# Optimization experiments

Hardware: AMD Instinct MI355X
Metric: run time of the kernel (lower is better)

## Reference

```python
import jax, jax.numpy as jnp
import numpy as np

N_NODES = 100000


def setup_inputs() -> dict:
    key = jax.random.key(0)
    k1, k2, k3, k4, k5 = jax.random.split(key, 5)
    n_edges = 3200000
    in_f, out_f = 256, 256
    X = jax.random.normal(k1, (N_NODES, in_f), dtype=jnp.float32)
    edge_src = jax.random.randint(k2, (n_edges,), 0, N_NODES, dtype=jnp.int32)
    edge_dst = jax.random.randint(k3, (n_edges,), 0, N_NODES, dtype=jnp.int32)
    edge_val = jax.random.uniform(k4, (n_edges,), dtype=jnp.float32)
    # kaiming-uniform-like init for weight (out_f, in_f)
    bound = np.sqrt(6.0 / in_f)
    W = jax.random.uniform(k5, (out_f, in_f), dtype=jnp.float32, minval=-bound, maxval=bound)
    b = jnp.zeros((out_f,), dtype=jnp.float32)
    return {"X": X, "edge_src": edge_src, "edge_dst": edge_dst,
            "edge_val": edge_val, "W": W, "b": b}


def reference(X, edge_src, edge_dst, edge_val, W, b):
    # S = A @ X, where A is COO sparse: A[src, dst] = val
    # gather neighbor features, scale by edge value, scatter-add to src rows
    msgs = edge_val[:, None] * X[edge_dst]              # [E, in_f]
    S = jax.ops.segment_sum(msgs, edge_src, num_segments=N_NODES)  # [N, in_f]
    # dense projection + bias: (A X) W^T + b
    return S @ W.T + b
```

## Files before the change

kernel.cpp:

```cpp
#include <hip/hip_runtime.h>

#define NNODES 100000
#define F 256
#define NBKT ((NNODES + 127) / 128)
#define BKT_CAP 5120
#define CHUNK_A 8192

typedef unsigned short u16;
typedef unsigned int   u32;
typedef __attribute__((ext_vector_type(8))) short short8v;
typedef __attribute__((ext_vector_type(8))) unsigned short ushort8;
typedef __attribute__((ext_vector_type(4))) float f32x4;
typedef __attribute__((ext_vector_type(2))) float f32x2;

#define GLDS(g, l) __builtin_amdgcn_global_load_lds(                                \
    (const __attribute__((address_space(1))) void*)(g),                             \
    (__attribute__((address_space(3))) void*)(l), 16, 0, 0)

__device__ __forceinline__ u16 f2bf(float f) {
    u32 u = __float_as_uint(f);
    u32 r = u + 0x7FFFu + ((u >> 16) & 1u);
    return (u16)(r >> 16);
}

__global__ __launch_bounds__(256) void cast_w_init(const float* __restrict__ W,
                                                   u16* __restrict__ Wb,
                                                   int* __restrict__ cur) {
    int i = blockIdx.x * 256 + threadIdx.x;
    if (i < F * F / 4) {
        float4 w = ((const float4*)W)[i];
        ushort4 o;
        o.x = f2bf(w.x); o.y = f2bf(w.y); o.z = f2bf(w.z); o.w = f2bf(w.w);
        ((ushort4*)Wb)[i] = o;
    }
    if (i < NBKT) cur[i] = i * BKT_CAP;
}

__global__ __launch_bounds__(256) void cast_x(const float* __restrict__ X,
                                              u16* __restrict__ Xb, int total4) {
    int i = blockIdx.x * 256 + threadIdx.x;
    if (i >= total4) return;
    float4 x = ((const float4*)X)[i];
    ushort4 o;
    o.x = f2bf(x.x); o.y = f2bf(x.y); o.z = f2bf(x.z); o.w = f2bf(x.w);
    ((ushort4*)Xb)[i] = o;
}

__global__ __launch_bounds__(256) void gemm_mfma(const u16* __restrict__ Xb,
                                                 const u16* __restrict__ Wb,
                                                 u16* __restrict__ Yb) {
    __shared__ u16 As[128 * 128];
    __shared__ u16 Bs[128 * 128];
    const int tid  = threadIdx.x;
    const int wv   = tid >> 6;
    const int lane = tid & 63;
    const int lm   = lane & 15;
    const int kg   = lane >> 4;
    const int m0   = blockIdx.x * 128;
    const int n0   = blockIdx.y * 128;

    const u32 csb = (u32)(((tid & 15) ^ ((tid >> 4) & 7)) * 16);
    const u32 rbb = (u32)((tid >> 4) * 512);
    const char* gA0 = (const char*)Xb + (size_t)m0 * 512 + rbb + csb;
    const char* gB0 = (const char*)Wb + (size_t)n0 * 512 + rbb + csb;
    const u32 wbase = (u32)(wv * 1024);

    f32x4 acc[2][8];
#pragma unroll
    for (int t = 0; t < 2; ++t)
#pragma unroll
        for (int u = 0; u < 8; ++u) acc[t][u] = (f32x4){0.f, 0.f, 0.f, 0.f};

#pragma unroll
    for (int kt = 0; kt < 2; ++kt) {
        if (kt) __syncthreads();
#pragma unroll
        for (int i = 0; i < 8; ++i) {
            GLDS(gA0 + kt * 256 + i * 8192, (char*)As + i * 4096 + wbase);
            GLDS(gB0 + kt * 256 + i * 8192, (char*)Bs + i * 4096 + wbase);
        }
        __syncthreads();
#pragma unroll
        for (int s = 0; s < 4; ++s) {
            short8v aF[2];
#pragma unroll
            for (int t = 0; t < 2; ++t) {
                int r = wv * 32 + t * 16 + lm;
                int c = (s * 4 + kg) ^ (r & 7);
                aF[t] = *(const short8v*)&As[r * 128 + c * 8];
            }
            short8v bF[8];
#pragma unroll
            for (int u = 0; u < 8; ++u) {
                int r = u * 16 + lm;
                int c = (s * 4 + kg) ^ (r & 7);
                bF[u] = *(const short8v*)&Bs[r * 128 + c * 8];
            }
#pragma unroll
            for (int t = 0; t < 2; ++t)
#pragma unroll
                for (int u = 0; u < 8; ++u)
                    acc[t][u] = __builtin_amdgcn_mfma_f32_16x16x32_bf16(aF[t], bF[u], acc[t][u], 0, 0, 0);
        }
    }

#pragma unroll
    for (int t = 0; t < 2; ++t) {
        int rbase = m0 + wv * 32 + t * 16 + kg * 4;
#pragma unroll
        for (int i = 0; i < 4; ++i) {
            int row = rbase + i;
            if (row < NNODES) {
#pragma unroll
                for (int u = 0; u < 8; ++u)
                    Yb[(size_t)row * F + n0 + u * 16 + lm] = f2bf(acc[t][u][i]);
            }
        }
    }
}

__global__ __launch_bounds__(256) void bin_edges(const int* __restrict__ src,
                                                 const int* __restrict__ dst,
                                                 const float* __restrict__ val,
                                                 int* __restrict__ cur,
                                                 int2* __restrict__ temp,
                                                 int n_edges) {
    __shared__ int hist[NBKT];
    __shared__ int bas[NBKT];
    const int e0 = blockIdx.x * CHUNK_A;
    for (int i = threadIdx.x; i < NBKT; i += 256) hist[i] = 0;
    __syncthreads();

    u32 lpk[32];
#pragma unroll
    for (int k = 0; k < 32; ++k) {
        int e = e0 + k * 256 + threadIdx.x;
        if (e < n_edges) {
            int s = src[e];
            int bkt = s >> 7;
            int l = atomicAdd(&hist[bkt], 1);
            lpk[k] = (u32)l | ((u32)(s & 127) << 13) | ((u32)bkt << 20);
        }
    }
    __syncthreads();
    for (int i = threadIdx.x; i < NBKT; i += 256) {
        int c = hist[i];
        bas[i] = c ? atomicAdd(&cur[i], c) : 0;
    }
    __syncthreads();
#pragma unroll
    for (int k = 0; k < 32; ++k) {
        int e = e0 + k * 256 + threadIdx.x;
        if (e < n_edges) {
            u32 p   = lpk[k];
            int bkt = (int)(p >> 20);
            int pos = bas[bkt] + (int)(p & 0x1FFFu);
            int sl  = (int)((p >> 13) & 127u);
            temp[pos] = make_int2((sl << 20) | dst[e], __float_as_int(val[e]));
        }
    }
}

__global__ __launch_bounds__(256) void sort_bucket(const int* __restrict__ cur,
                                                   const int2* __restrict__ temp,
                                                   int2* __restrict__ pack,
                                                   int2* __restrict__ nodeseg) {
    __shared__ int2 tl[BKT_CAP];
    __shared__ int h[128];
    __shared__ int curl[128];
    const int b = blockIdx.x;
    const int base = b * BKT_CAP;
    int cnt = cur[b] - base;
    if (cnt > BKT_CAP) cnt = BKT_CAP;
    const int tid = threadIdx.x;

    if (tid < 128) h[tid] = 0;
    __syncthreads();
    for (int j = tid; j < cnt; j += 256) {
        int2 t = temp[base + j];
        tl[j] = t;
        atomicAdd(&h[t.x >> 20], 1);
    }
    __syncthreads();
    for (int off = 1; off < 128; off <<= 1) {
        int x = 0;
        if (tid < 128 && tid >= off) x = h[tid - off];
        __syncthreads();
        if (tid < 128) h[tid] += x;
        __syncthreads();
    }
    if (tid < 128) {
        int incl = h[tid];
        int prev = tid ? h[tid - 1] : 0;
        curl[tid] = base + prev;
        int node = b * 128 + tid;
        if (node < NNODES) nodeseg[node] = make_int2(base + prev, base + incl);
    }
    __syncthreads();
    for (int j = tid; j < cnt; j += 256) {
        int2 p = tl[j];
        int loc = p.x >> 20;
        int pos = atomicAdd(&curl[loc], 1);
        pack[pos] = make_int2((p.x & 0xFFFFF) << 9, p.y);
    }
}

__global__ __launch_bounds__(256) void gather_nodes(const int2* __restrict__ nodeseg,
                                                    const int2* __restrict__ pack,
                                                    const u16* __restrict__ Yb,
                                                    const float* __restrict__ bias,
                                                    float* __restrict__ out) {
    int node = blockIdx.x * 4 + (threadIdx.x >> 6);
    if (node >= NNODES) return;
    const int lane = threadIdx.x & 63;
    const int half = lane >> 5;
    const int l5   = lane & 31;
    const u32 loff = (u32)l5 * 16u;
    const char* Ybc = (const char*)Yb;

    int2 seg = nodeseg[node];
    const int beg = seg.x, end = seg.y;

    f32x2 acc2[4];
#pragma unroll
    for (int i = 0; i < 4; ++i) acc2[i] = (f32x2){0.f, 0.f};

    for (int j = beg; j < end; j += 16) {
        u32 off[8];
        float v[8];
        ushort8 y[8];
#pragma unroll
        for (int q = 0; q < 8; ++q) {
            int idx = j + 2 * q + half;
            int safe = idx < end ? idx : end - 1;
            long long raw = __builtin_nontemporal_load((const long long*)&pack[safe]);
            off[q] = (u32)((unsigned long long)raw & 0xFFFFFFFFull);
            v[q] = (idx < end) ? __int_as_float((int)(raw >> 32)) : 0.f;
        }
#pragma unroll
        for (int q = 0; q < 8; ++q)
            y[q] = *(const ushort8*)(Ybc + (off[q] + loff));
#pragma unroll
        for (int q = 0; q < 8; ++q) {
            f32x2 vv; vv[0] = v[q]; vv[1] = v[q];
            const u32* yp = (const u32*)&y[q];
#pragma unroll
            for (int i = 0; i < 4; ++i) {
                u32 pb = yp[i];
                f32x2 yy;
                yy[0] = __uint_as_float(pb << 16);
                yy[1] = __uint_as_float(pb & 0xFFFF0000u);
                acc2[i] = __builtin_elementwise_fma(yy, vv, acc2[i]);
            }
        }
    }

    float acc[8];
#pragma unroll
    for (int i = 0; i < 4; ++i) { acc[2 * i] = acc2[i][0]; acc[2 * i + 1] = acc2[i][1]; }
#pragma unroll
    for (int i = 0; i < 8; ++i) acc[i] += __shfl_xor(acc[i], 32);

    const int col = l5 * 8 + half * 4;
    float4 bv = *(const float4*)&bias[col];
    f32x4 o;
    o[0] = acc[half * 4 + 0] + bv.x;
    o[1] = acc[half * 4 + 1] + bv.y;
    o[2] = acc[half * 4 + 2] + bv.z;
    o[3] = acc[half * 4 + 3] + bv.w;
    __builtin_nontemporal_store(o, (f32x4*)&out[(size_t)node * F + col]);
}

extern "C" void kernel_launch(void* const* d_in, const int* in_sizes, int n_in,
                              void* d_out, int out_size, void* d_ws, size_t ws_size,
                              hipStream_t stream) {
    const float* X        = (const float*)d_in[0];
    const int*   edge_src = (const int*)d_in[1];
    const int*   edge_dst = (const int*)d_in[2];
    const float* edge_val = (const float*)d_in[3];
    const float* W        = (const float*)d_in[4];
    const float* b        = (const float*)d_in[5];
    float*       out      = (float*)d_out;
    const int n_edges     = in_sizes[1];

    char* base = (char*)d_ws;
    const size_t ybBytes   = (size_t)NNODES * F * sizeof(u16);
    const size_t packBytes = (size_t)NBKT * BKT_CAP * sizeof(int2);
    u16*  Yb      = (u16*)base;
    int2* pack    = (int2*)(base + ybBytes);
    int2* temp    = (int2*)(base + ybBytes + packBytes);
    u16*  Xb      = (u16*)pack;
    u16*  Wb      = (u16*)(base + ybBytes + 2 * packBytes);
    int2* nodeseg = (int2*)((char*)Wb + (size_t)F * F * sizeof(u16));
    int*  cur     = (int*)(nodeseg + NNODES);

    cast_w_init<<<(F * F / 4 + 255) / 256, 256, 0, stream>>>(W, Wb, cur);
    int xt4 = NNODES * F / 4;
    cast_x<<<(xt4 + 255) / 256, 256, 0, stream>>>(X, Xb, xt4);

    dim3 ggrid((NNODES + 127) / 128, F / 128);
    gemm_mfma<<<ggrid, 256, 0, stream>>>(Xb, Wb, Yb);

    bin_edges<<<(n_edges + CHUNK_A - 1) / CHUNK_A, 256, 0, stream>>>(edge_src, edge_dst, edge_val,
                                                                     cur, temp, n_edges);
    sort_bucket<<<NBKT, 256, 0, stream>>>(cur, temp, pack, nodeseg);

    gather_nodes<<<(NNODES + 3) / 4, 256, 0, stream>>>(nodeseg, pack, Yb, b, out);
}
```

Baseline: 555.9 us.

## Fuse bucket sort and node gather into one kernel using LDS-resident edges

```diff
diff --git a/kernel.cpp b/kernel.cpp
--- a/kernel.cpp
+++ b/kernel.cpp
@@ -3,7 +3,7 @@
 #define NNODES 100000
 #define F 256
 #define NBKT ((NNODES + 127) / 128)
-#define BKT_CAP 5120
+#define BKT_CAP 5040
 #define CHUNK_A 8192
 
 typedef unsigned short u16;
@@ -156,30 +156,38 @@
             int bkt = (int)(p >> 20);
             int pos = bas[bkt] + (int)(p & 0x1FFFu);
             int sl  = (int)((p >> 13) & 127u);
-            temp[pos] = make_int2((sl << 20) | dst[e], __float_as_int(val[e]));
-        }
-    }
-}
-
-__global__ __launch_bounds__(256) void sort_bucket(const int* __restrict__ cur,
+            if (pos < (bkt + 1) * BKT_CAP)
+                temp[pos] = make_int2((sl << 20) | dst[e], __float_as_int(val[e]));
+        }
+    }
+}
+
+__global__ __launch_bounds__(256) void sort_gather(const int* __restrict__ cur,
                                                    const int2* __restrict__ temp,
-                                                   int2* __restrict__ pack,
-                                                   int2* __restrict__ nodeseg) {
-    __shared__ int2 tl[BKT_CAP];
+                                                   const u16* __restrict__ Yb,
+                                                   const float* __restrict__ bias,
+                                                   float* __restrict__ out) {
+    __shared__ int2 pk[BKT_CAP];
     __shared__ int h[128];
-    __shared__ int curl[128];
     const int b = blockIdx.x;
     const int base = b * BKT_CAP;
+    const int tid = threadIdx.x;
     int cnt = cur[b] - base;
     if (cnt > BKT_CAP) cnt = BKT_CAP;
-    const int tid = threadIdx.x;
 
     if (tid < 128) h[tid] = 0;
     __syncthreads();
-    for (int j = tid; j < cnt; j += 256) {
-        int2 t = temp[base + j];
-        tl[j] = t;
-        atomicAdd(&h[t.x >> 20], 1);
+
+    int2 ed[20];
+    int  lp[20];
+#pragma unroll
+    for (int q = 0; q < 20; ++q) {
+        int j = q * 256 + tid;
+        if (j < cnt) {
+            int2 t = temp[base + j];
+            ed[q] = t;
+            lp[q] = atomicAdd(&h[t.x >> 20], 1);
+        }
     }
     __syncthreads();
     for (int off = 1; off < 128; off <<= 1) {
@@ -189,86 +197,80 @@
         if (tid < 128) h[tid] += x;
         __syncthreads();
     }
-    if (tid < 128) {
-        int incl = h[tid];
-        int prev = tid ? h[tid - 1] : 0;
-        curl[tid] = base + prev;
-        int node = b * 128 + tid;
-        if (node < NNODES) nodeseg[node] = make_int2(base + prev, base + incl);
-    }
-    __syncthreads();
-    for (int j = tid; j < cnt; j += 256) {
-        int2 p = tl[j];
-        int loc = p.x >> 20;
-        int pos = atomicAdd(&curl[loc], 1);
-        pack[pos] = make_int2((p.x & 0xFFFFF) << 9, p.y);
-    }
-}
-
-__global__ __launch_bounds__(256) void gather_nodes(const int2* __restrict__ nodeseg,
-                                                    const int2* __restrict__ pack,
-                                                    const u16* __restrict__ Yb,
-                                                    const float* __restrict__ bias,
-                                                    float* __restrict__ out) {
-    int node = blockIdx.x * 4 + (threadIdx.x >> 6);
-    if (node >= NNODES) return;
-    const int lane = threadIdx.x & 63;
+#pragma unroll
+    for (int q = 0; q < 20; ++q) {
+        int j = q * 256 + tid;
+        if (j < cnt) {
+            int loc = ed[q].x >> 20;
+            int st  = loc ? h[loc - 1] : 0;
+            pk[st + lp[q]] = make_int2((ed[q].x & 0xFFFFF) << 9, ed[q].y);
+        }
+    }
+    __syncthreads();
+
+    const int wv   = tid >> 6;
+    const int lane = tid & 63;
     const int half = lane >> 5;
     const int l5   = lane & 31;
     const u32 loff = (u32)l5 * 16u;
     const char* Ybc = (const char*)Yb;
-
-    int2 seg = nodeseg[node];
-    const int beg = seg.x, end = seg.y;
-
-    f32x2 acc2[4];
-#pragma unroll
-    for (int i = 0; i < 4; ++i) acc2[i] = (f32x2){0.f, 0.f};
-
-    for (int j = beg; j < end; j += 16) {
-        u32 off[8];
-        float v[8];
-        ushort8 y[8];
-#pragma unroll
-        for (int q = 0; q < 8; ++q) {
-            int idx = j + 2 * q + half;
-            int safe = idx < end ? idx : end - 1;
-            long long raw = __builtin_nontemporal_load((const long long*)&pack[safe]);
-            off[q] = (u32)((unsigned long long)raw & 0xFFFFFFFFull);
-            v[q] = (idx < end) ? __int_as_float((int)(raw >> 32)) : 0.f;
-        }
-#pragma unroll
-        for (int q = 0; q < 8; ++q)
-            y[q] = *(const ushort8*)(Ybc + (off[q] + loff));
-#pragma unroll
-        for (int q = 0; q < 8; ++q) {
-            f32x2 vv; vv[0] = v[q]; vv[1] = v[q];
-            const u32* yp = (const u32*)&y[q];
-#pragma unroll
-            for (int i = 0; i < 4; ++i) {
-                u32 pb = yp[i];
-                f32x2 yy;
-                yy[0] = __uint_as_float(pb << 16);
-                yy[1] = __uint_as_float(pb & 0xFFFF0000u);
-                acc2[i] = __builtin_elementwise_fma(yy, vv, acc2[i]);
-            }
-        }
-    }
-
-    float acc[8];
-#pragma unroll
-    for (int i = 0; i < 4; ++i) { acc[2 * i] = acc2[i][0]; acc[2 * i + 1] = acc2[i][1]; }
-#pragma unroll
-    for (int i = 0; i < 8; ++i) acc[i] += __shfl_xor(acc[i], 32);
-
     const int col = l5 * 8 + half * 4;
-    float4 bv = *(const float4*)&bias[col];
-    f32x4 o;
-    o[0] = acc[half * 4 + 0] + bv.x;
-    o[1] = acc[half * 4 + 1] + bv.y;
-    o[2] = acc[half * 4 + 2] + bv.z;
-    o[3] = acc[half * 4 + 3] + bv.w;
-    __builtin_nontemporal_store(o, (f32x4*)&out[(size_t)node * F + col]);
+    const float4 bv = *(const float4*)&bias[col];
+
+    for (int k = 0; k < 32; ++k) {
+        int ln   = wv * 32 + k;
+        int node = b * 128 + ln;
+        if (node >= NNODES) break;
+        int beg = ln ? h[ln - 1] : 0;
+        int end = h[ln];
+
+        f32x2 acc2[4];
+#pragma unroll
+        for (int i = 0; i < 4; ++i) acc2[i] = (f32x2){0.f, 0.f};
+
+        for (int j = beg; j < end; j += 16) {
+            u32 off8[8];
+            float v[8];
+            ushort8 y[8];
+#pragma unroll
+            for (int q = 0; q < 8; ++q) {
+                int idx  = j + 2 * q + half;
+                int safe = idx < end ? idx : end - 1;
+                int2 p = pk[safe];
+                off8[q] = (u32)p.x;
+                v[q]    = (idx < end) ? __int_as_float(p.y) : 0.f;
+            }
+#pragma unroll
+            for (int q = 0; q < 8; ++q)
+                y[q] = *(const ushort8*)(Ybc + (off8[q] + loff));
+#pragma unroll
+            for (int q = 0; q < 8; ++q) {
+                f32x2 vv; vv[0] = v[q]; vv[1] = v[q];
+                const u32* yp = (const u32*)&y[q];
+#pragma unroll
+                for (int i = 0; i < 4; ++i) {
+                    u32 pb = yp[i];
+                    f32x2 yy;
+                    yy[0] = __uint_as_float(pb << 16);
+                    yy[1] = __uint_as_float(pb & 0xFFFF0000u);
+                    acc2[i] = __builtin_elementwise_fma(yy, vv, acc2[i]);
+                }
+            }
+        }
+
+        float acc[8];
+#pragma unroll
+        for (int i = 0; i < 4; ++i) { acc[2 * i] = acc2[i][0]; acc[2 * i + 1] = acc2[i][1]; }
+#pragma unroll
+        for (int i = 0; i < 8; ++i) acc[i] += __shfl_xor(acc[i], 32);
+
+        f32x4 o;
+        o[0] = acc[half * 4 + 0] + bv.x;
+        o[1] = acc[half * 4 + 1] + bv.y;
+        o[2] = acc[half * 4 + 2] + bv.z;
+        o[3] = acc[half * 4 + 3] + bv.w;
+        __builtin_nontemporal_store(o, (f32x4*)&out[(size_t)node * F + col]);
+    }
 }
 
 extern "C" void kernel_launch(void* const* d_in, const int* in_sizes, int n_in,
@@ -285,14 +287,12 @@
 
     char* base = (char*)d_ws;
     const size_t ybBytes   = (size_t)NNODES * F * sizeof(u16);
-    const size_t packBytes = (size_t)NBKT * BKT_CAP * sizeof(int2);
+    const size_t xbBytes   = (size_t)100096 * F * sizeof(u16);
     u16*  Yb      = (u16*)base;
-    int2* pack    = (int2*)(base + ybBytes);
-    int2* temp    = (int2*)(base + ybBytes + packBytes);
-    u16*  Xb      = (u16*)pack;
-    u16*  Wb      = (u16*)(base + ybBytes + 2 * packBytes);
-    int2* nodeseg = (int2*)((char*)Wb + (size_t)F * F * sizeof(u16));
-    int*  cur     = (int*)(nodeseg + NNODES);
+    int2* temp    = (int2*)(base + ybBytes);
+    u16*  Xb      = (u16*)temp;
+    u16*  Wb      = (u16*)(base + ybBytes + xbBytes);
+    int*  cur     = (int*)((char*)Wb + (size_t)F * F * sizeof(u16));
 
     cast_w_init<<<(F * F / 4 + 255) / 256, 256, 0, stream>>>(W, Wb, cur);
     int xt4 = NNODES * F / 4;
@@ -303,7 +303,6 @@
 
     bin_edges<<<(n_edges + CHUNK_A - 1) / CHUNK_A, 256, 0, stream>>>(edge_src, edge_dst, edge_val,
                                                                      cur, temp, n_edges);
-    sort_bucket<<<NBKT, 256, 0, stream>>>(cur, temp, pack, nodeseg);
-
-    gather_nodes<<<(NNODES + 3) / 4, 256, 0, stream>>>(nodeseg, pack, Yb, b, out);
-}
+
+    sort_gather<<<NBKT, 256, 0, stream>>>(cur, temp, Yb, b, out);
+}
```

New measurement: 575.2 us. 1.03x slower.
